# Performance work log

Hardware: AMD Instinct MI355X
Metric: run time of the kernel (lower is better)

Reference implementation:

```python
import jax, jax.numpy as jnp
import numpy as np

LN_EPS = 1e-5

def setup_inputs() -> dict:
    key = jax.random.key(0)
    k1, k2, k3 = jax.random.split(key, 3)
    B, Lq, Lk, D = 16, 2048, 2048, 128
    return {
        "query": jax.random.normal(k1, (B, Lq, D), dtype=jnp.float32),
        "key": jax.random.normal(k2, (B, Lk, D), dtype=jnp.float32),
        "value": jax.random.normal(k3, (B, Lk, D), dtype=jnp.float32),
        "attn_mask": jnp.zeros((Lq, Lk), dtype=jnp.float32),
        "gamma": jnp.ones((D,), dtype=jnp.float32),
        "beta": jnp.zeros((D,), dtype=jnp.float32),
    }

def reference(query, key, value, attn_mask, gamma, beta):
    # NOTE: original code does NOT scale by 1/sqrt(d) despite the class name.
    scores = jnp.einsum("bqd,bkd->bqk", query, key)          # [B,Lq,Lk]
    scores = scores + attn_mask[None, :, :]
    probs = jax.nn.softmax(scores, axis=-1)
    out = jnp.einsum("bqk,bkd->bqd", probs, value)            # [B,Lq,D]
    # dropout is identity (eval / rate 0)
    mu = jnp.mean(out, axis=-1, keepdims=True)
    var = jnp.var(out, axis=-1, keepdims=True)
    normed = (out - mu) * jax.lax.rsqrt(var + LN_EPS)
    return normed * gamma + beta
```

## Files before the change

kernel.cpp:

```cpp
#include <hip/hip_runtime.h>
#include <hip/hip_bf16.h>
#include <math.h>

#define LQ_  2048
#define LK_  2048
#define D_   128
#define B_   16
#define LN_EPS 1e-5f
#define TK_  32
#define NTILE (LK_ / TK_)

#define KH_TILE_US 4096
#define VT_TILE_U  2560
#define KH_BYTES   ((size_t)B_ * NTILE * KH_TILE_US * 2)
#define VT_OFF     (2 * KH_BYTES)

typedef __attribute__((ext_vector_type(8))) short short8;
typedef __attribute__((ext_vector_type(4))) float f32x4;

union FragU { uint4 u4; short8 s8; unsigned int u[4]; };

__device__ __forceinline__ unsigned int pk_bf16(float a, float b) {
  __hip_bfloat162 h = __float22bfloat162_rn(make_float2(a, b));
  unsigned int u;
  __builtin_memcpy(&u, &h, 4);
  return u;
}
__device__ __forceinline__ float bf_lo(unsigned int u){ unsigned int v = u << 16; float f; __builtin_memcpy(&f, &v, 4); return f; }
__device__ __forceinline__ float bf_hi(unsigned int u){ unsigned int v = u & 0xffff0000u; float f; __builtin_memcpy(&f, &v, 4); return f; }
__device__ __forceinline__ unsigned short bf16_bits(float x) {
  return (unsigned short)(pk_bf16(x, 0.f) & 0xffffu);
}

__device__ __forceinline__ int idxK(int row, int d) {
  return row * 128 + ((((d >> 3) ^ row) & 15) << 3) + (d & 7);
}
__device__ __forceinline__ int idxVt(int d, int kp) {
  int h = ((d >> 2) ^ ((d & 3) << 1)) & 3;
  return d * 20 + ((((kp >> 2) ^ h) & 3) << 2) + (kp & 3);
}
__device__ __forceinline__ int idxPs(int row, int col) {
  return row * 32 + ((((col >> 3) ^ (row >> 2)) & 3) << 3) + (col & 7);
}

__device__ __forceinline__ void barrier_lds() {
  asm volatile("s_waitcnt lgkmcnt(0)\n\ts_barrier" ::: "memory");
}
__device__ __forceinline__ void barrier_stage() {
  asm volatile("s_waitcnt vmcnt(8) lgkmcnt(0)\n\ts_barrier" ::: "memory");
}

__device__ __forceinline__ void gld_lds16(const void* g, void* l) {
  __builtin_amdgcn_global_load_lds((const __attribute__((address_space(1))) void*)g,
                                   (__attribute__((address_space(3))) void*)l, 16, 0, 0);
}
__device__ __forceinline__ void gld_lds4(const void* g, void* l) {
  __builtin_amdgcn_global_load_lds((const __attribute__((address_space(1))) void*)g,
                                   (__attribute__((address_space(3))) void*)l, 4, 0, 0);
}

__global__ __launch_bounds__(256) void conv_kv(
    const float* __restrict__ kg, const float* __restrict__ vg,
    unsigned short* __restrict__ khg, unsigned short* __restrict__ klg,
    unsigned int* __restrict__ vtg)
{
  __shared__ float Vl[32 * 128];
  const int tid = threadIdx.x;
  const int blk = blockIdx.x;
  const int b = blk >> 6;
  const int t = blk & 63;

  const float* ks = kg + ((size_t)b * LK_ + t * 32) * D_;
  const float* vs = vg + ((size_t)b * LK_ + t * 32) * D_;
  unsigned short* kh = khg + (size_t)blk * KH_TILE_US;
  unsigned short* kl = klg + (size_t)blk * KH_TILE_US;
  unsigned int*   vt = vtg + (size_t)blk * VT_TILE_U;

#pragma unroll
  for (int it = 0; it < 2; it++) {
    const int item = tid + it * 256;
    const int row = item >> 4;
    const int c8  = item & 15;
    const float* p = ks + row * D_ + c8 * 8;
    float4 x = *(const float4*)(p);
    float4 y = *(const float4*)(p + 4);
    FragU H, L;
    H.u[0] = pk_bf16(x.x, x.y); H.u[1] = pk_bf16(x.z, x.w);
    H.u[2] = pk_bf16(y.x, y.y); H.u[3] = pk_bf16(y.z, y.w);
    L.u[0] = pk_bf16(x.x - bf_lo(H.u[0]), x.y - bf_hi(H.u[0]));
    L.u[1] = pk_bf16(x.z - bf_lo(H.u[1]), x.w - bf_hi(H.u[1]));
    L.u[2] = pk_bf16(y.x - bf_lo(H.u[2]), y.y - bf_hi(H.u[2]));
    L.u[3] = pk_bf16(y.z - bf_lo(H.u[3]), y.w - bf_hi(H.u[3]));
    const int ik = idxK(row, c8 * 8);
    *(uint4*)&kh[ik] = H.u4;
    *(uint4*)&kl[ik] = L.u4;
  }

#pragma unroll
  for (int i = 0; i < 4; i++) {
    const int item = tid + i * 256;
    *(float4*)&Vl[item * 4] = *(const float4*)&vs[item * 4];
  }
  __syncthreads();

#pragma unroll
  for (int i = 0; i < 10; i++) {
    const int o = tid + i * 256;
    const int d = o / 20;
    const int slot = o - d * 20;
    unsigned int val = 0u;
    if (slot < 16) {
      const int g = slot >> 2, c = slot & 3;
      const int h = ((d >> 2) ^ ((d & 3) << 1)) & 3;
      const int kp = (((g ^ h) & 3) << 2) | c;
      val = pk_bf16(Vl[(2 * kp) * D_ + d], Vl[(2 * kp + 1) * D_ + d]);
    }
    vt[o] = val;
  }
}

__device__ __forceinline__ void stage_tile(int w, int lane,
    const unsigned short* khT, const unsigned short* klT, const unsigned int* vtT,
    int tile, unsigned short* khs, unsigned short* kls, unsigned int* vts)
{
  const char* gkh = (const char*)(khT + (size_t)tile * KH_TILE_US);
  const char* gkl = (const char*)(klT + (size_t)tile * KH_TILE_US);
  const char* gvt = (const char*)(vtT + (size_t)tile * VT_TILE_U);
#pragma unroll
  for (int c = 0; c < 2; c++) {
    const int off = (w + 4 * c) << 10;
    gld_lds16(gkh + off + lane * 16, (char*)khs + off);
    gld_lds16(gkl + off + lane * 16, (char*)kls + off);
    gld_lds16(gvt + off + lane * 16, (char*)vts + off);
  }
#pragma unroll
  for (int c = 0; c < 2; c++) {
    const int off = 8192 + ((w + 4 * c) << 8);
    gld_lds4(gvt + off + lane * 4, (char*)vts + off);
  }
}

__global__ __launch_bounds__(256, 2) void attn_ln_mfma(
    const float* __restrict__ qg, const float* __restrict__ maskg,
    const float* __restrict__ gammag, const float* __restrict__ betag,
    const unsigned short* __restrict__ khg, const unsigned short* __restrict__ klg,
    const unsigned int* __restrict__ vtg,
    float* __restrict__ outg)
{
  __shared__ unsigned short KhS[2][32 * 128];
  __shared__ unsigned short KlS[2][32 * 128];
  __shared__ unsigned int   VtW[2][128 * 20];
  __shared__ unsigned short PsS[64 * 32];
  __shared__ float lExch[2 * 64];
  __shared__ float sExch[2 * 64 * 2];

  const int tid  = threadIdx.x;
  const int w    = tid >> 6;
  const int lane = tid & 63;
  const int quad = lane >> 4;
  const int lr   = lane & 15;
  const int rowgrp = w & 1;
  const int khalf  = w >> 1;

  const int id   = blockIdx.x;
  const int xcd  = id & 7;
  const int slot = id >> 3;
  const int b    = xcd * 2 + (slot >> 5);
  const int q0   = (slot & 31) * 64;

  const unsigned short* khT = khg + (size_t)b * NTILE * KH_TILE_US;
  const unsigned short* klT = klg + (size_t)b * NTILE * KH_TILE_US;
  const unsigned int*   vtT = vtg + (size_t)b * NTILE * VT_TILE_U;

  stage_tile(w, lane, khT, klT, vtT, 0, &KhS[0][0], &KlS[0][0], &VtW[0][0]);

  short8 qh[2][4], ql[2][4];
#pragma unroll
  for (int rt = 0; rt < 2; rt++) {
    const float* qrow = qg + ((size_t)b * LQ_ + q0 + rowgrp * 32 + rt * 16 + lr) * D_ + quad * 8;
#pragma unroll
    for (int c = 0; c < 4; c++) {
      float4 x = *(const float4*)(qrow + c * 32);
      float4 y = *(const float4*)(qrow + c * 32 + 4);
      FragU H, L;
      H.u[0] = pk_bf16(x.x, x.y); H.u[1] = pk_bf16(x.z, x.w);
      H.u[2] = pk_bf16(y.x, y.y); H.u[3] = pk_bf16(y.z, y.w);
      L.u[0] = pk_bf16(x.x - bf_lo(H.u[0]), x.y - bf_hi(H.u[0]));
      L.u[1] = pk_bf16(x.z - bf_lo(H.u[1]), x.w - bf_hi(H.u[1]));
      L.u[2] = pk_bf16(y.x - bf_lo(H.u[2]), y.y - bf_hi(H.u[2]));
      L.u[3] = pk_bf16(y.z - bf_lo(H.u[3]), y.w - bf_hi(H.u[3]));
      qh[rt][c] = H.s8; ql[rt][c] = L.s8;
    }
  }

  float l_part[2][4];
  f32x4 o[2][4];
  const f32x4 zf = {0.f, 0.f, 0.f, 0.f};
#pragma unroll
  for (int rt = 0; rt < 2; rt++) {
#pragma unroll
    for (int r = 0; r < 4; r++) l_part[rt][r] = 0.f;
#pragma unroll
    for (int n = 0; n < 4; n++) o[rt][n] = zf;
  }

  const float* mbase = maskg + (size_t)(q0 + rowgrp * 32 + quad * 4) * LK_ + khalf * 16 + lr;

  for (int kt = 0; kt < NTILE; kt++) {
    const int cur = kt & 1;
    const unsigned short* khc = &KhS[cur][0];
    const unsigned short* klc = &KlS[cur][0];
    const unsigned int*   vtc = &VtW[cur][0];

    float mkv[2][4];
#pragma unroll
    for (int rt = 0; rt < 2; rt++)
#pragma unroll
      for (int reg = 0; reg < 4; reg++)
        mkv[rt][reg] = mbase[(size_t)(rt * 16 + reg) * LK_ + kt * TK_];

    barrier_stage();

    if (kt + 1 < NTILE)
      stage_tile(w, lane, khT, klT, vtT, kt + 1,
                 &KhS[cur ^ 1][0], &KlS[cur ^ 1][0], &VtW[cur ^ 1][0]);

    f32x4 sacc[2];
    sacc[0] = zf; sacc[1] = zf;
#pragma unroll
    for (int c = 0; c < 4; c++) {
      const int kb = c * 32 + quad * 8;
      const int krow = khalf * 16 + lr;
      FragU kh, kl;
      kh.u4 = *(const uint4*)&khc[idxK(krow, kb)];
      kl.u4 = *(const uint4*)&klc[idxK(krow, kb)];
#pragma unroll
      for (int rt = 0; rt < 2; rt++) {
        sacc[rt] = __builtin_amdgcn_mfma_f32_16x16x32_bf16(qh[rt][c], kh.s8, sacc[rt], 0, 0, 0);
        sacc[rt] = __builtin_amdgcn_mfma_f32_16x16x32_bf16(ql[rt][c], kh.s8, sacc[rt], 0, 0, 0);
        sacc[rt] = __builtin_amdgcn_mfma_f32_16x16x32_bf16(qh[rt][c], kl.s8, sacc[rt], 0, 0, 0);
      }
    }

#pragma unroll
    for (int rt = 0; rt < 2; rt++)
#pragma unroll
      for (int reg = 0; reg < 4; reg++) {
        float p = __expf(sacc[rt][reg] + mkv[rt][reg]);
        l_part[rt][reg] += p;
        PsS[idxPs(rowgrp * 32 + rt * 16 + quad * 4 + reg, khalf * 16 + lr)] = bf16_bits(p);
      }

    barrier_lds();

    FragU Bv[4];
#pragma unroll
    for (int nb = 0; nb < 4; nb++)
      Bv[nb].u4 = *(const uint4*)&vtc[idxVt(khalf * 64 + nb * 16 + lr, quad * 4)];
#pragma unroll
    for (int rt = 0; rt < 2; rt++) {
      FragU A;
      A.u4 = *(const uint4*)&PsS[idxPs(rowgrp * 32 + rt * 16 + lr, quad * 8)];
#pragma unroll
      for (int nb = 0; nb < 4; nb++)
        o[rt][nb] = __builtin_amdgcn_mfma_f32_16x16x32_bf16(A.s8, Bv[nb].s8, o[rt][nb], 0, 0, 0);
    }
  }

  float lred[2][4];
#pragma unroll
  for (int rt = 0; rt < 2; rt++)
#pragma unroll
    for (int reg = 0; reg < 4; reg++) {
      float l = l_part[rt][reg];
#pragma unroll
      for (int m = 1; m <= 8; m <<= 1) l += __shfl_xor(l, m, 64);
      lred[rt][reg] = l;
    }
  if (lr == 0) {
#pragma unroll
    for (int rt = 0; rt < 2; rt++)
#pragma unroll
      for (int reg = 0; reg < 4; reg++)
        lExch[khalf * 64 + rowgrp * 32 + rt * 16 + quad * 4 + reg] = lred[rt][reg];
  }
  barrier_lds();

  float inv_l[2][4];
#pragma unroll
  for (int rt = 0; rt < 2; rt++)
#pragma unroll
    for (int reg = 0; reg < 4; reg++) {
      const int row = rowgrp * 32 + rt * 16 + quad * 4 + reg;
      inv_l[rt][reg] = 1.f / (lred[rt][reg] + lExch[(1 ^ khalf) * 64 + row]);
    }

  float s1p[2][4], s2p[2][4];
#pragma unroll
  for (int rt = 0; rt < 2; rt++)
#pragma unroll
    for (int reg = 0; reg < 4; reg++) {
      float s1 = 0.f, s2 = 0.f;
#pragma unroll
      for (int nb = 0; nb < 4; nb++) {
        float v = o[rt][nb][reg] * inv_l[rt][reg];
        o[rt][nb][reg] = v;
        s1 += v; s2 += v * v;
      }
#pragma unroll
      for (int m = 1; m <= 8; m <<= 1) {
        s1 += __shfl_xor(s1, m, 64);
        s2 += __shfl_xor(s2, m, 64);
      }
      s1p[rt][reg] = s1; s2p[rt][reg] = s2;
    }
  if (lr == 0) {
#pragma unroll
    for (int rt = 0; rt < 2; rt++)
#pragma unroll
      for (int reg = 0; reg < 4; reg++) {
        const int row = rowgrp * 32 + rt * 16 + quad * 4 + reg;
        sExch[(khalf * 64 + row) * 2 + 0] = s1p[rt][reg];
        sExch[(khalf * 64 + row) * 2 + 1] = s2p[rt][reg];
      }
  }
  barrier_lds();

  float gam[4], bet[4];
#pragma unroll
  for (int nb = 0; nb < 4; nb++) {
    gam[nb] = gammag[khalf * 64 + nb * 16 + lr];
    bet[nb] = betag[khalf * 64 + nb * 16 + lr];
  }

#pragma unroll
  for (int rt = 0; rt < 2; rt++)
#pragma unroll
    for (int reg = 0; reg < 4; reg++) {
      const int row = rowgrp * 32 + rt * 16 + quad * 4 + reg;
      const float s1 = s1p[rt][reg] + sExch[((1 ^ khalf) * 64 + row) * 2 + 0];
      const float s2 = s2p[rt][reg] + sExch[((1 ^ khalf) * 64 + row) * 2 + 1];
      const float mean = s1 * (1.f / 128.f);
      const float var  = s2 * (1.f / 128.f) - mean * mean;
      const float rstd = rsqrtf(var + LN_EPS);

      float* op = outg + ((size_t)b * LQ_ + q0 + row) * D_ + khalf * 64 + lr;
#pragma unroll
      for (int nb = 0; nb < 4; nb++)
        op[nb * 16] = (o[rt][nb][reg] - mean) * rstd * gam[nb] + bet[nb];
    }
}

extern "C" void kernel_launch(void* const* d_in, const int* in_sizes, int n_in,
                              void* d_out, int out_size, void* d_ws, size_t ws_size,
                              hipStream_t stream) {
  const float* q     = (const float*)d_in[0];
  const float* k     = (const float*)d_in[1];
  const float* v     = (const float*)d_in[2];
  const float* mask  = (const float*)d_in[3];
  const float* gamma = (const float*)d_in[4];
  const float* beta  = (const float*)d_in[5];
  float* out = (float*)d_out;

  unsigned short* khg = (unsigned short*)d_ws;
  unsigned short* klg = (unsigned short*)((char*)d_ws + KH_BYTES);
  unsigned int*   vtg = (unsigned int*)((char*)d_ws + VT_OFF);

  conv_kv<<<dim3(B_ * NTILE), dim3(256), 0, stream>>>(k, v, khg, klg, vtg);
  attn_ln_mfma<<<dim3(512), dim3(256), 0, stream>>>(q, mask, gamma, beta,
                                                    khg, klg, vtg, out);
}
```

Before: 214.8 us.

## Compact V tile LDS layout, raise occupancy, prefetch mask one tile ahead

Shrinks the transposed V tile from a padded 20-word row stride to 16 words, using a rotation swizzle instead of padding to avoid bank conflicts. This removes the extra 4-byte global-to-LDS loads, and the conv kernel now transposes V through a padded shared buffer. Reusing the P scratch buffer for the row-sum and stats exchange frees enough LDS to raise launch bounds from 2 to 3 blocks per CU. The mask values are now prefetched one tile ahead and the V fragment loads are moved before the softmax barrier to hide latency. The costs are tighter register limits at 3 blocks per CU and an added barrier before the epilogue.

```diff
diff --git a/kernel.cpp b/kernel.cpp
--- a/kernel.cpp
+++ b/kernel.cpp
@@ -11,7 +11,7 @@
 #define NTILE (LK_ / TK_)
 
 #define KH_TILE_US 4096
-#define VT_TILE_U  2560
+#define VT_TILE_U  2048
 #define KH_BYTES   ((size_t)B_ * NTILE * KH_TILE_US * 2)
 #define VT_OFF     (2 * KH_BYTES)
 
@@ -36,8 +36,7 @@
   return row * 128 + ((((d >> 3) ^ row) & 15) << 3) + (d & 7);
 }
 __device__ __forceinline__ int idxVt(int d, int kp) {
-  int h = ((d >> 2) ^ ((d & 3) << 1)) & 3;
-  return d * 20 + ((((kp >> 2) ^ h) & 3) << 2) + (kp & 3);
+  return d * 16 + ((((kp >> 2) + (d >> 1)) & 3) << 2) + (kp & 3);
 }
 __device__ __forceinline__ int idxPs(int row, int col) {
   return row * 32 + ((((col >> 3) ^ (row >> 2)) & 3) << 3) + (col & 7);
@@ -53,10 +52,6 @@
 __device__ __forceinline__ void gld_lds16(const void* g, void* l) {
   __builtin_amdgcn_global_load_lds((const __attribute__((address_space(1))) void*)g,
                                    (__attribute__((address_space(3))) void*)l, 16, 0, 0);
-}
-__device__ __forceinline__ void gld_lds4(const void* g, void* l) {
-  __builtin_amdgcn_global_load_lds((const __attribute__((address_space(1))) void*)g,
-                                   (__attribute__((address_space(3))) void*)l, 4, 0, 0);
 }
 
 __global__ __launch_bounds__(256) void conv_kv(
@@ -64,7 +59,7 @@
     unsigned short* __restrict__ khg, unsigned short* __restrict__ klg,
     unsigned int* __restrict__ vtg)
 {
-  __shared__ float Vl[32 * 128];
+  __shared__ float Vlt[128 * 33];
   const int tid = threadIdx.x;
   const int blk = blockIdx.x;
   const int b = blk >> 6;
@@ -99,23 +94,22 @@
 #pragma unroll
   for (int i = 0; i < 4; i++) {
     const int item = tid + i * 256;
-    *(float4*)&Vl[item * 4] = *(const float4*)&vs[item * 4];
+    const int r = item >> 5, c4 = item & 31;
+    float4 x = *(const float4*)&vs[r * D_ + c4 * 4];
+    Vlt[(c4 * 4 + 0) * 33 + r] = x.x;
+    Vlt[(c4 * 4 + 1) * 33 + r] = x.y;
+    Vlt[(c4 * 4 + 2) * 33 + r] = x.z;
+    Vlt[(c4 * 4 + 3) * 33 + r] = x.w;
   }
   __syncthreads();
 
 #pragma unroll
-  for (int i = 0; i < 10; i++) {
+  for (int i = 0; i < 8; i++) {
     const int o = tid + i * 256;
-    const int d = o / 20;
-    const int slot = o - d * 20;
-    unsigned int val = 0u;
-    if (slot < 16) {
-      const int g = slot >> 2, c = slot & 3;
-      const int h = ((d >> 2) ^ ((d & 3) << 1)) & 3;
-      const int kp = (((g ^ h) & 3) << 2) | c;
-      val = pk_bf16(Vl[(2 * kp) * D_ + d], Vl[(2 * kp + 1) * D_ + d]);
-    }
-    vt[o] = val;
+    const int d = o >> 4, s = o & 15;
+    const int gq = s >> 2, c = s & 3;
+    const int kp = (((gq - (d >> 1)) & 3) << 2) | c;
+    vt[o] = pk_bf16(Vlt[d * 33 + 2 * kp], Vlt[d * 33 + 2 * kp + 1]);
   }
 }
 
@@ -133,14 +127,9 @@
     gld_lds16(gkl + off + lane * 16, (char*)kls + off);
     gld_lds16(gvt + off + lane * 16, (char*)vts + off);
   }
-#pragma unroll
-  for (int c = 0; c < 2; c++) {
-    const int off = 8192 + ((w + 4 * c) << 8);
-    gld_lds4(gvt + off + lane * 4, (char*)vts + off);
-  }
-}
-
-__global__ __launch_bounds__(256, 2) void attn_ln_mfma(
+}
+
+__global__ __launch_bounds__(256, 3) void attn_ln_mfma(
     const float* __restrict__ qg, const float* __restrict__ maskg,
     const float* __restrict__ gammag, const float* __restrict__ betag,
     const unsigned short* __restrict__ khg, const unsigned short* __restrict__ klg,
@@ -149,10 +138,11 @@
 {
   __shared__ unsigned short KhS[2][32 * 128];
   __shared__ unsigned short KlS[2][32 * 128];
-  __shared__ unsigned int   VtW[2][128 * 20];
+  __shared__ unsigned int   VtW[2][128 * 16];
   __shared__ unsigned short PsS[64 * 32];
-  __shared__ float lExch[2 * 64];
-  __shared__ float sExch[2 * 64 * 2];
+
+  float* lExch = (float*)&PsS[0];
+  float* sExch = ((float*)&PsS[0]) + 128;
 
   const int tid  = threadIdx.x;
   const int w    = tid >> 6;
@@ -172,7 +162,15 @@
   const unsigned short* klT = klg + (size_t)b * NTILE * KH_TILE_US;
   const unsigned int*   vtT = vtg + (size_t)b * NTILE * VT_TILE_U;
 
+  const float* mbase = maskg + (size_t)(q0 + rowgrp * 32 + quad * 4) * LK_ + khalf * 16 + lr;
+
   stage_tile(w, lane, khT, klT, vtT, 0, &KhS[0][0], &KlS[0][0], &VtW[0][0]);
+  float mcur[2][4];
+#pragma unroll
+  for (int rt = 0; rt < 2; rt++)
+#pragma unroll
+    for (int reg = 0; reg < 4; reg++)
+      mcur[rt][reg] = mbase[(size_t)(rt * 16 + reg) * LK_];
 
   short8 qh[2][4], ql[2][4];
 #pragma unroll
@@ -204,26 +202,24 @@
     for (int n = 0; n < 4; n++) o[rt][n] = zf;
   }
 
-  const float* mbase = maskg + (size_t)(q0 + rowgrp * 32 + quad * 4) * LK_ + khalf * 16 + lr;
-
   for (int kt = 0; kt < NTILE; kt++) {
     const int cur = kt & 1;
     const unsigned short* khc = &KhS[cur][0];
     const unsigned short* klc = &KlS[cur][0];
     const unsigned int*   vtc = &VtW[cur][0];
 
-    float mkv[2][4];
-#pragma unroll
-    for (int rt = 0; rt < 2; rt++)
-#pragma unroll
-      for (int reg = 0; reg < 4; reg++)
-        mkv[rt][reg] = mbase[(size_t)(rt * 16 + reg) * LK_ + kt * TK_];
-
     barrier_stage();
 
-    if (kt + 1 < NTILE)
+    float mnext[2][4];
+    if (kt + 1 < NTILE) {
       stage_tile(w, lane, khT, klT, vtT, kt + 1,
                  &KhS[cur ^ 1][0], &KlS[cur ^ 1][0], &VtW[cur ^ 1][0]);
+#pragma unroll
+      for (int rt = 0; rt < 2; rt++)
+#pragma unroll
+        for (int reg = 0; reg < 4; reg++)
+          mnext[rt][reg] = mbase[(size_t)(rt * 16 + reg) * LK_ + (kt + 1) * TK_];
+    }
 
     f32x4 sacc[2];
     sacc[0] = zf; sacc[1] = zf;
@@ -242,21 +238,22 @@
       }
     }
 
+    FragU Bv[4];
+#pragma unroll
+    for (int nb = 0; nb < 4; nb++)
+      Bv[nb].u4 = *(const uint4*)&vtc[idxVt(khalf * 64 + nb * 16 + lr, quad * 4)];
+
 #pragma unroll
     for (int rt = 0; rt < 2; rt++)
 #pragma unroll
       for (int reg = 0; reg < 4; reg++) {
-        float p = __expf(sacc[rt][reg] + mkv[rt][reg]);
+        float p = __expf(sacc[rt][reg] + mcur[rt][reg]);
         l_part[rt][reg] += p;
         PsS[idxPs(rowgrp * 32 + rt * 16 + quad * 4 + reg, khalf * 16 + lr)] = bf16_bits(p);
       }
 
     barrier_lds();
 
-    FragU Bv[4];
-#pragma unroll
-    for (int nb = 0; nb < 4; nb++)
-      Bv[nb].u4 = *(const uint4*)&vtc[idxVt(khalf * 64 + nb * 16 + lr, quad * 4)];
 #pragma unroll
     for (int rt = 0; rt < 2; rt++) {
       FragU A;
@@ -265,7 +262,17 @@
       for (int nb = 0; nb < 4; nb++)
         o[rt][nb] = __builtin_amdgcn_mfma_f32_16x16x32_bf16(A.s8, Bv[nb].s8, o[rt][nb], 0, 0, 0);
     }
-  }
+
+    if (kt + 1 < NTILE) {
+#pragma unroll
+      for (int rt = 0; rt < 2; rt++)
+#pragma unroll
+        for (int reg = 0; reg < 4; reg++)
+          mcur[rt][reg] = mnext[rt][reg];
+    }
+  }
+
+  barrier_lds();
 
   float lred[2][4];
 #pragma unroll
```

Result: slower. 243.4 us (+13.3%).
